# Optimization experiments

Hardware: AMD Instinct MI355X
Metric: run time of the kernel (lower is better)

Reference implementation:

```python
import jax, jax.numpy as jnp
import numpy as np

N = 50000      # nodes
E = 800000     # edges
IN = 128       # in_channels
C = 32         # hidden_channels per head
H = 8          # heads
NC = 2         # num_classes
EPS = 1e-5     # batchnorm eps
SLOPE = 0.2    # leaky relu negative slope


def setup_inputs() -> dict:
    key = jax.random.key(0)
    ks = jax.random.split(key, 16)
    d = {}
    d["x"] = jax.random.normal(ks[0], (N, IN), dtype=jnp.float32)
    d["edge_index"] = jax.random.randint(ks[1], (2, E), 0, N, dtype=jnp.int64)
    # layer 0: IN -> H*C (concat)
    s0 = 1.0 / np.sqrt(IN)
    d["Wl0"] = jax.random.normal(ks[2], (IN, H * C), dtype=jnp.float32) * s0
    d["Wr0"] = jax.random.normal(ks[3], (IN, H * C), dtype=jnp.float32) * s0
    d["att0"] = jax.random.normal(ks[4], (H, C), dtype=jnp.float32) * (1.0 / np.sqrt(C))
    d["b0"] = jnp.zeros((H * C,), dtype=jnp.float32)
    d["g0"] = jnp.ones((H * C,), dtype=jnp.float32)
    d["be0"] = jnp.zeros((H * C,), dtype=jnp.float32)
    d["m0"] = jax.random.normal(ks[5], (H * C,), dtype=jnp.float32) * 0.1
    d["v0"] = jax.random.uniform(ks[6], (H * C,), dtype=jnp.float32, minval=0.5, maxval=1.5)
    # layer 1: H*C -> C (mean over heads, concat=False)
    s1 = 1.0 / np.sqrt(H * C)
    d["Wl1"] = jax.random.normal(ks[7], (H * C, H * C), dtype=jnp.float32) * s1
    d["Wr1"] = jax.random.normal(ks[8], (H * C, H * C), dtype=jnp.float32) * s1
    d["att1"] = jax.random.normal(ks[9], (H, C), dtype=jnp.float32) * (1.0 / np.sqrt(C))
    d["b1"] = jnp.zeros((C,), dtype=jnp.float32)
    d["g1"] = jnp.ones((C,), dtype=jnp.float32)
    d["be1"] = jnp.zeros((C,), dtype=jnp.float32)
    d["m1"] = jax.random.normal(ks[10], (C,), dtype=jnp.float32) * 0.1
    d["v1"] = jax.random.uniform(ks[11], (C,), dtype=jnp.float32, minval=0.5, maxval=1.5)
    # classifier C -> NC
    d["Wc"] = jax.random.normal(ks[12], (C, NC), dtype=jnp.float32) * (1.0 / np.sqrt(C))
    d["bc"] = jnp.zeros((NC,), dtype=jnp.float32)
    return d


def _gatv2_layer(x, src, dst, Wl, Wr, att, b, concat, num_nodes):
    # GATv2Conv (PyG semantics): x_l = source proj, x_r = target proj,
    # e_ij = att . LeakyReLU(x_l[j] + x_r[i]); softmax over incoming edges of i;
    # out_i = sum_j alpha_ij * x_l[j]. Self-loops are added (PyG default).
    nH, nC = att.shape
    xl = (x @ Wl).reshape(num_nodes, nH, nC)
    xr = (x @ Wr).reshape(num_nodes, nH, nC)
    e = xl[src] + xr[dst]                              # [E', H, C]
    e = jnp.where(e > 0, e, SLOPE * e)
    logits = jnp.einsum('ehc,hc->eh', e, att)          # [E', H]
    m = jax.ops.segment_max(logits, dst, num_segments=num_nodes)   # [N, H]
    ex = jnp.exp(logits - m[dst])
    denom = jax.ops.segment_sum(ex, dst, num_segments=num_nodes)   # [N, H]
    alpha = ex / denom[dst]                            # [E', H]
    msg = alpha[:, :, None] * xl[src]                  # [E', H, C]
    out = jax.ops.segment_sum(msg, dst, num_segments=num_nodes)    # [N, H, C]
    if concat:
        return out.reshape(num_nodes, nH * nC) + b
    return out.mean(axis=1) + b


def _bn(x, g, be, m, v):
    return (x - m) * jax.lax.rsqrt(v + EPS) * g + be


def reference(x, edge_index, Wl0, Wr0, att0, b0, g0, be0, m0, v0,
              Wl1, Wr1, att1, b1, g1, be1, m1, v1, Wc, bc):
    num_nodes = x.shape[0]
    loop = jnp.arange(num_nodes, dtype=edge_index.dtype)
    src = jnp.concatenate([edge_index[0], loop])
    dst = jnp.concatenate([edge_index[1], loop])
    h = _gatv2_layer(x, src, dst, Wl0, Wr0, att0, b0, True, num_nodes)
    h = _bn(h, g0, be0, m0, v0)
    h = jax.nn.elu(h)   # eval mode: dropout is identity
    h = _gatv2_layer(h, src, dst, Wl1, Wr1, att1, b1, False, num_nodes)
    h = _bn(h, g1, be1, m1, v1)
    return h @ Wc + bc
```

## Files before the change

kernel.cpp:

```cpp
#include <hip/hip_runtime.h>
#include <math.h>

#define N_NODES 50000
#define M_PAD   50048
#define E_EDGES 800000
#define IN_CH   128
#define C_CH    32
#define H_HEADS 8
#define HC      256
#define BN_EPS  1e-5f
#define SLOPE   0.2f

#define SCAN_CHUNK 512
#define SCAN_B     ((N_NODES + SCAN_CHUNK - 1) / SCAN_CHUNK)

typedef _Float16 f16x8 __attribute__((ext_vector_type(8)));
typedef _Float16 f16x4 __attribute__((ext_vector_type(4)));
typedef _Float16 f16x2 __attribute__((ext_vector_type(2)));
typedef float    f32x4 __attribute__((ext_vector_type(4)));


__global__ void k_init_deg(int* deg, int n) {
    int i = blockIdx.x * blockDim.x + threadIdx.x;
    if (i < n) deg[i] = 1;
}

__global__ void k_hist(const int* __restrict__ dst, int* deg, int e) {
    int i = blockIdx.x * blockDim.x + threadIdx.x;
    if (i < e) atomicAdd(&deg[dst[i]], 1);
}

__global__ __launch_bounds__(256) void k_scan_local(
        const int* __restrict__ deg, int* __restrict__ row_ptr,
        int* __restrict__ partials, int n) {
    __shared__ int sm[256];
    int t = threadIdx.x;
    int base = blockIdx.x * SCAN_CHUNK;
    int i0 = base + 2 * t, i1 = i0 + 1;
    int a = (i0 < n) ? deg[i0] : 0;
    int b = (i1 < n) ? deg[i1] : 0;
    int s = a + b;
    sm[t] = s;
    __syncthreads();
    #pragma unroll
    for (int off = 1; off < 256; off <<= 1) {
        int u = (t >= off) ? sm[t - off] : 0;
        __syncthreads();
        sm[t] += u;
        __syncthreads();
    }
    int excl = sm[t] - s;
    if (i0 < n) row_ptr[i0] = excl;
    if (i1 < n) row_ptr[i1] = excl + a;
    if (t == 255) partials[blockIdx.x] = sm[255];
}

__global__ __launch_bounds__(128) void k_scan_part(
        int* __restrict__ partials, int* __restrict__ row_ptr_n) {
    __shared__ int sm[128];
    int t = threadIdx.x;
    int v = (t < SCAN_B) ? partials[t] : 0;
    sm[t] = v;
    __syncthreads();
    #pragma unroll
    for (int off = 1; off < 128; off <<= 1) {
        int u = (t >= off) ? sm[t - off] : 0;
        __syncthreads();
        sm[t] += u;
        __syncthreads();
    }
    if (t < SCAN_B) partials[t] = sm[t] - v;
    if (t == 127) *row_ptr_n = sm[127];
}

__global__ void k_scan_add(int* __restrict__ row_ptr, int* __restrict__ cursor,
                           const int* __restrict__ partials, int n) {
    int i = blockIdx.x * blockDim.x + threadIdx.x;
    if (i < n) {
        int v = row_ptr[i] + partials[i / SCAN_CHUNK];
        row_ptr[i] = v;
        cursor[i] = v;
    }
}

__global__ void k_fill(const int* __restrict__ src, const int* __restrict__ dst,
                       int* cursor, int* csr_src, int e, int n) {
    int i = blockIdx.x * blockDim.x + threadIdx.x;
    if (i < e) {
        int d = dst[i];
        int p = atomicAdd(&cursor[d], 1);
        csr_src[p] = src[i];
    } else if (i < e + n) {
        int v = i - e;
        int p = atomicAdd(&cursor[v], 1);
        csr_src[p] = v;
    }
}


__global__ void k_split_w4(const float* __restrict__ Wl0, const float* __restrict__ Wr0,
                           const float* __restrict__ Wl1, const float* __restrict__ Wr1,
                           _Float16* __restrict__ W0lt, _Float16* __restrict__ W0rt,
                           _Float16* __restrict__ W1lt, _Float16* __restrict__ W1rt) {
    int t = blockIdx.x * blockDim.x + threadIdx.x;
    const float* W; _Float16* O; int K, rel;
    if (t < 32768)       { W = Wl0; O = W0lt; K = 128; rel = t; }
    else if (t < 65536)  { W = Wr0; O = W0rt; K = 128; rel = t - 32768; }
    else if (t < 131072) { W = Wl1; O = W1lt; K = 256; rel = t - 65536; }
    else if (t < 196608) { W = Wr1; O = W1rt; K = 256; rel = t - 131072; }
    else return;
    int n = rel / K, k = rel - n * K;
    O[rel] = (_Float16)W[(size_t)k * 256 + n];
}


#define BK  32
#define LDA 40

__device__ __forceinline__ f16x8 cvt_h8(float4 a, float4 b) {
    f16x8 v = { (_Float16)a.x, (_Float16)a.y, (_Float16)a.z, (_Float16)a.w,
                (_Float16)b.x, (_Float16)b.y, (_Float16)b.z, (_Float16)b.w };
    return v;
}

__global__ __launch_bounds__(256) void k_gemm_mfma(
        const _Float16* __restrict__ A16, const float* __restrict__ A32,
        const _Float16* __restrict__ W0t, const _Float16* __restrict__ W1t,
        _Float16* __restrict__ C0, _Float16* __restrict__ C1, int K) {
    const _Float16* Wt = blockIdx.z ? W1t : W0t;
    _Float16* C = blockIdx.z ? C1 : C0;
    __shared__ _Float16 As[128 * LDA];
    __shared__ _Float16 Bs[128 * LDA];
    int t = threadIdx.x;
    int lane = t & 63, wv = t >> 6;
    int quad = lane >> 4, r16 = lane & 15;
    size_t mBase = (size_t)blockIdx.x * 128;
    size_t nBase = (size_t)blockIdx.y * 128;
    int sr = t >> 2;
    int sc = (t & 3) * 8;
    f32x4 acc[2][8] = {};
    for (int k0 = 0; k0 < K; k0 += BK) {
        if (A32) {
            size_t r0 = mBase + sr, r1 = r0 + 64;
            float4 a0 = {0.f,0.f,0.f,0.f}, a1 = a0, b0 = a0, b1 = a0;
            if (r0 < N_NODES) {
                const float* g = A32 + r0 * K + k0 + sc;
                a0 = ((const float4*)g)[0];
                a1 = ((const float4*)g)[1];
            }
            if (r1 < N_NODES) {
                const float* g = A32 + r1 * K + k0 + sc;
                b0 = ((const float4*)g)[0];
                b1 = ((const float4*)g)[1];
            }
            *(f16x8*)&As[sr * LDA + sc]        = cvt_h8(a0, a1);
            *(f16x8*)&As[(sr + 64) * LDA + sc] = cvt_h8(b0, b1);
        } else {
            const _Float16* gA = A16 + (mBase + sr) * K + k0 + sc;
            *(f16x8*)&As[sr * LDA + sc]        = *(const f16x8*)gA;
            *(f16x8*)&As[(sr + 64) * LDA + sc] = *(const f16x8*)(gA + (size_t)64 * K);
        }
        const _Float16* gB = Wt + (nBase + sr) * K + k0 + sc;
        *(f16x8*)&Bs[sr * LDA + sc]        = *(const f16x8*)gB;
        *(f16x8*)&Bs[(sr + 64) * LDA + sc] = *(const f16x8*)(gB + (size_t)64 * K);
        __syncthreads();
        f16x8 av[2];
        #pragma unroll
        for (int mi = 0; mi < 2; ++mi) {
            int m = wv * 32 + mi * 16 + r16;
            av[mi] = *(f16x8*)&As[m * LDA + quad * 8];
        }
        #pragma unroll
        for (int ni = 0; ni < 8; ++ni) {
            int n = ni * 16 + r16;
            f16x8 bv = *(f16x8*)&Bs[n * LDA + quad * 8];
            #pragma unroll
            for (int mi = 0; mi < 2; ++mi)
                acc[mi][ni] = __builtin_amdgcn_mfma_f32_16x16x32_f16(av[mi], bv, acc[mi][ni], 0, 0, 0);
        }
        __syncthreads();
    }
    #pragma unroll
    for (int mi = 0; mi < 2; ++mi)
        #pragma unroll
        for (int r = 0; r < 4; ++r) {
            size_t row = mBase + wv * 32 + mi * 16 + quad * 4 + r;
            _Float16* cp = C + row * 256 + nBase + r16;
            #pragma unroll
            for (int ni = 0; ni < 8; ++ni)
                cp[ni * 16] = (_Float16)acc[mi][ni][r];
        }
}


__device__ __forceinline__ float edge_w16(f16x4 h, f16x4 xr, f16x4 att) {
    f16x4 e = h + xr;
    f16x4 es = e * (_Float16)SLOPE;
    f16x4 l = __builtin_elementwise_max(e, es);
#if __has_builtin(__builtin_amdgcn_fdot2)
    f16x2 l01 = __builtin_shufflevector(l, l, 0, 1);
    f16x2 l23 = __builtin_shufflevector(l, l, 2, 3);
    f16x2 a01 = __builtin_shufflevector(att, att, 0, 1);
    f16x2 a23 = __builtin_shufflevector(att, att, 2, 3);
    float p = __builtin_amdgcn_fdot2(l01, a01, 0.f, false);
    p = __builtin_amdgcn_fdot2(l23, a23, p, false);
#else
    float p = (float)l[0] * (float)att[0];
    p = fmaf((float)l[1], (float)att[1], p);
    p = fmaf((float)l[2], (float)att[2], p);
    p = fmaf((float)l[3], (float)att[3], p);
#endif
    p += __shfl_xor(p, 1);
    p += __shfl_xor(p, 2);
    p += __shfl_xor(p, 4);
    return __expf(p);
}

__device__ __forceinline__ float4 edge_accum(
        const f16x4* __restrict__ xl4, f16x4 xr_h, f16x4 att_h,
        const int* __restrict__ csr_src, int beg, int end, int lane) {
    const f16x4* xlp = xl4 + lane;
    float4 acc = {0.f, 0.f, 0.f, 0.f};
    float S = 0.f;
    int j = beg;
    for (; j + 4 <= end; j += 4) {
        int s0 = csr_src[j];
        int s1 = csr_src[j + 1];
        int s2 = csr_src[j + 2];
        int s3 = csr_src[j + 3];
        f16x4 h0 = xlp[(size_t)s0 * 64];
        f16x4 h1 = xlp[(size_t)s1 * 64];
        f16x4 h2 = xlp[(size_t)s2 * 64];
        f16x4 h3 = xlp[(size_t)s3 * 64];
        float w0 = edge_w16(h0, xr_h, att_h);
        float w1 = edge_w16(h1, xr_h, att_h);
        float w2 = edge_w16(h2, xr_h, att_h);
        float w3 = edge_w16(h3, xr_h, att_h);
        S += (w0 + w1) + (w2 + w3);
        acc.x = fmaf((float)h0[0], w0, acc.x); acc.y = fmaf((float)h0[1], w0, acc.y);
        acc.z = fmaf((float)h0[2], w0, acc.z); acc.w = fmaf((float)h0[3], w0, acc.w);
        acc.x = fmaf((float)h1[0], w1, acc.x); acc.y = fmaf((float)h1[1], w1, acc.y);
        acc.z = fmaf((float)h1[2], w1, acc.z); acc.w = fmaf((float)h1[3], w1, acc.w);
        acc.x = fmaf((float)h2[0], w2, acc.x); acc.y = fmaf((float)h2[1], w2, acc.y);
        acc.z = fmaf((float)h2[2], w2, acc.z); acc.w = fmaf((float)h2[3], w2, acc.w);
        acc.x = fmaf((float)h3[0], w3, acc.x); acc.y = fmaf((float)h3[1], w3, acc.y);
        acc.z = fmaf((float)h3[2], w3, acc.z); acc.w = fmaf((float)h3[3], w3, acc.w);
    }
    for (; j < end; ++j) {
        int s = csr_src[j];
        f16x4 hv = xlp[(size_t)s * 64];
        float w = edge_w16(hv, xr_h, att_h);
        S += w;
        acc.x = fmaf((float)hv[0], w, acc.x); acc.y = fmaf((float)hv[1], w, acc.y);
        acc.z = fmaf((float)hv[2], w, acc.z); acc.w = fmaf((float)hv[3], w, acc.w);
    }
    float inv = 1.f / S;
    acc.x *= inv; acc.y *= inv; acc.z *= inv; acc.w *= inv;
    return acc;
}

__device__ __forceinline__ f16x4 cvt_h4(float4 v) {
    f16x4 r = { (_Float16)v.x, (_Float16)v.y, (_Float16)v.z, (_Float16)v.w };
    return r;
}

__global__ __launch_bounds__(256) void k_edge0(
        const _Float16* __restrict__ xl, const _Float16* __restrict__ xr,
        const float* __restrict__ att,
        const int* __restrict__ row_ptr, const int* __restrict__ csr_src,
        const float* __restrict__ b0, const float* __restrict__ g0,
        const float* __restrict__ be0, const float* __restrict__ m0,
        const float* __restrict__ v0,
        _Float16* __restrict__ h0) {
    int lane = threadIdx.x & 63;
    int i = blockIdx.x * 4 + (threadIdx.x >> 6);
    const f16x4* xl4 = (const f16x4*)xl;
    f16x4 xr_h = ((const f16x4*)xr)[(size_t)i * 64 + lane];
    f16x4 att_h = cvt_h4(((const float4*)att)[lane]);
    int beg = row_ptr[i], end = row_ptr[i + 1];
    float4 r = edge_accum(xl4, xr_h, att_h, csr_src, beg, end, lane);
    float4 bb = ((const float4*)b0)[lane];
    float4 gg = ((const float4*)g0)[lane];
    float4 ee = ((const float4*)be0)[lane];
    float4 mm = ((const float4*)m0)[lane];
    float4 vv = ((const float4*)v0)[lane];
    float4 o;
    o.x = (r.x + bb.x - mm.x) * rsqrtf(vv.x + BN_EPS) * gg.x + ee.x;
    o.y = (r.y + bb.y - mm.y) * rsqrtf(vv.y + BN_EPS) * gg.y + ee.y;
    o.z = (r.z + bb.z - mm.z) * rsqrtf(vv.z + BN_EPS) * gg.z + ee.z;
    o.w = (r.w + bb.w - mm.w) * rsqrtf(vv.w + BN_EPS) * gg.w + ee.w;
    o.x = o.x > 0.f ? o.x : expm1f(o.x);
    o.y = o.y > 0.f ? o.y : expm1f(o.y);
    o.z = o.z > 0.f ? o.z : expm1f(o.z);
    o.w = o.w > 0.f ? o.w : expm1f(o.w);
    f16x4 hh = { (_Float16)o.x, (_Float16)o.y, (_Float16)o.z, (_Float16)o.w };
    ((f16x4*)h0)[(size_t)i * 64 + lane] = hh;
}

__global__ __launch_bounds__(256) void k_edge1(
        const _Float16* __restrict__ xl, const _Float16* __restrict__ xr,
        const float* __restrict__ att,
        const int* __restrict__ row_ptr, const int* __restrict__ csr_src,
        const float* __restrict__ b1, const float* __restrict__ g1,
        const float* __restrict__ be1, const float* __restrict__ m1,
        const float* __restrict__ v1,
        const float* __restrict__ Wc, const float* __restrict__ bc,
        float* __restrict__ out) {
    int lane = threadIdx.x & 63;
    int q = lane & 7;
    int i = blockIdx.x * 4 + (threadIdx.x >> 6);
    const f16x4* xl4 = (const f16x4*)xl;
    f16x4 xr_h = ((const f16x4*)xr)[(size_t)i * 64 + lane];
    f16x4 att_h = cvt_h4(((const float4*)att)[lane]);
    int beg = row_ptr[i], end = row_ptr[i + 1];
    float4 r = edge_accum(xl4, xr_h, att_h, csr_src, beg, end, lane);
    #pragma unroll
    for (int mask = 8; mask <= 32; mask <<= 1) {
        r.x += __shfl_xor(r.x, mask);
        r.y += __shfl_xor(r.y, mask);
        r.z += __shfl_xor(r.z, mask);
        r.w += __shfl_xor(r.w, mask);
    }
    float4 bb = ((const float4*)b1)[q];
    float4 gg = ((const float4*)g1)[q];
    float4 ee = ((const float4*)be1)[q];
    float4 mm = ((const float4*)m1)[q];
    float4 vv = ((const float4*)v1)[q];
    r.x = (r.x * 0.125f + bb.x - mm.x) * rsqrtf(vv.x + BN_EPS) * gg.x + ee.x;
    r.y = (r.y * 0.125f + bb.y - mm.y) * rsqrtf(vv.y + BN_EPS) * gg.y + ee.y;
    r.z = (r.z * 0.125f + bb.z - mm.z) * rsqrtf(vv.z + BN_EPS) * gg.z + ee.z;
    r.w = (r.w * 0.125f + bb.w - mm.w) * rsqrtf(vv.w + BN_EPS) * gg.w + ee.w;
    float4 wc0 = ((const float4*)Wc)[q * 2];
    float4 wc1 = ((const float4*)Wc)[q * 2 + 1];
    float o0 = r.x * wc0.x + r.y * wc0.z + r.z * wc1.x + r.w * wc1.z;
    float o1 = r.x * wc0.y + r.y * wc0.w + r.z * wc1.y + r.w * wc1.w;
    #pragma unroll
    for (int mask = 1; mask <= 4; mask <<= 1) {
        o0 += __shfl_xor(o0, mask);
        o1 += __shfl_xor(o1, mask);
    }
    if (lane == 0) {
        float2 ov = {o0 + bc[0], o1 + bc[1]};
        *(float2*)(out + (size_t)i * 2) = ov;
    }
}


extern "C" void kernel_launch(void* const* d_in, const int* in_sizes, int n_in,
                              void* d_out, int out_size, void* d_ws, size_t ws_size,
                              hipStream_t stream) {
    const float* x    = (const float*)d_in[0];
    const int*   ei   = (const int*)d_in[1];
    const float* Wl0  = (const float*)d_in[2];
    const float* Wr0  = (const float*)d_in[3];
    const float* att0 = (const float*)d_in[4];
    const float* b0   = (const float*)d_in[5];
    const float* g0   = (const float*)d_in[6];
    const float* be0  = (const float*)d_in[7];
    const float* m0   = (const float*)d_in[8];
    const float* v0   = (const float*)d_in[9];
    const float* Wl1  = (const float*)d_in[10];
    const float* Wr1  = (const float*)d_in[11];
    const float* att1 = (const float*)d_in[12];
    const float* b1   = (const float*)d_in[13];
    const float* g1   = (const float*)d_in[14];
    const float* be1  = (const float*)d_in[15];
    const float* m1   = (const float*)d_in[16];
    const float* v1   = (const float*)d_in[17];
    const float* Wc   = (const float*)d_in[18];
    const float* bc   = (const float*)d_in[19];
    float* out = (float*)d_out;

    const int N = N_NODES, E = E_EDGES;
    const int* srcp = ei;
    const int* dstp = ei + E;

    char* p = (char*)d_ws;
    _Float16* xlf = (_Float16*)p; p += (size_t)M_PAD * HC * 2;
    _Float16* xrf = (_Float16*)p; p += (size_t)M_PAD * HC * 2;
    _Float16* h0  = (_Float16*)p; p += (size_t)M_PAD * HC * 2;
    _Float16* W0lt = (_Float16*)p; p += (size_t)HC * IN_CH * 2;
    _Float16* W0rt = (_Float16*)p; p += (size_t)HC * IN_CH * 2;
    _Float16* W1lt = (_Float16*)p; p += (size_t)HC * HC * 2;
    _Float16* W1rt = (_Float16*)p; p += (size_t)HC * HC * 2;
    int* deg      = (int*)p;
    int* row_ptr  = deg + N;
    int* cursor   = row_ptr + (N + 1);
    int* partials = cursor + N;
    int* csr_src  = partials + ((SCAN_B + 3) & ~3);

    k_init_deg<<<(N + 255) / 256, 256, 0, stream>>>(deg, N);
    k_hist<<<(E + 255) / 256, 256, 0, stream>>>(dstp, deg, E);
    k_scan_local<<<SCAN_B, 256, 0, stream>>>(deg, row_ptr, partials, N);
    k_scan_part<<<1, 128, 0, stream>>>(partials, row_ptr + N);
    k_scan_add<<<(N + 255) / 256, 256, 0, stream>>>(row_ptr, cursor, partials, N);
    k_fill<<<(E + N + 255) / 256, 256, 0, stream>>>(srcp, dstp, cursor, csr_src, E, N);

    k_split_w4<<<768, 256, 0, stream>>>(Wl0, Wr0, Wl1, Wr1, W0lt, W0rt, W1lt, W1rt);

    dim3 ggrid(M_PAD / 128, 2, 2);
    k_gemm_mfma<<<ggrid, 256, 0, stream>>>(nullptr, x, W0lt, W0rt, xlf, xrf, IN_CH);
    k_edge0<<<N / 4, 256, 0, stream>>>(xlf, xrf, att0, row_ptr, csr_src,
                                       b0, g0, be0, m0, v0, h0);
    k_gemm_mfma<<<ggrid, 256, 0, stream>>>(h0, nullptr, W1lt, W1rt, xlf, xrf, HC);
    k_edge1<<<N / 4, 256, 0, stream>>>(xlf, xrf, att1, row_ptr, csr_src,
                                       b1, g1, be1, m1, v1, Wc, bc, out);
}
```

Baseline: 403.3 us.

## Fuse left/right GEMMs per block, persistent edge kernels, exp2 softmax with folded BN

The GEMM now computes both the left and right projections in one 512-thread block, so each A tile is loaded once and shared by two B tiles. Each wave owns 16 rows instead of 32. The edge kernels become grid-stride persistent loops over a fixed 2048 blocks, with BN scale and shift precomputed once per wave. The exponential switches to a native exp2, with log2e folded into the fp16 attention vector, and per-node index reads go through readfirstlane. Risks are lower per-wave MFMA reuse in the GEMM and small fp16 rounding differences from prescaling the attention vector.

Result: slower. 418.5 us (+3.8%).

```diff
diff --git a/kernel.cpp b/kernel.cpp
--- a/kernel.cpp
+++ b/kernel.cpp
@@ -10,14 +10,24 @@
 #define HC      256
 #define BN_EPS  1e-5f
 #define SLOPE   0.2f
+#define LOG2E   1.44269504f
 
 #define SCAN_CHUNK 512
 #define SCAN_B     ((N_NODES + SCAN_CHUNK - 1) / SCAN_CHUNK)
+
+#define EDGE_BLOCKS 2048
+#define EDGE_WAVES  (EDGE_BLOCKS * 4)
 
 typedef _Float16 f16x8 __attribute__((ext_vector_type(8)));
 typedef _Float16 f16x4 __attribute__((ext_vector_type(4)));
 typedef _Float16 f16x2 __attribute__((ext_vector_type(2)));
 typedef float    f32x4 __attribute__((ext_vector_type(4)));
+
+#if __has_builtin(__builtin_amdgcn_exp2f)
+#define EXP2F(x) __builtin_amdgcn_exp2f(x)
+#else
+#define EXP2F(x) exp2f(x)
+#endif
 
 
 __global__ void k_init_deg(int* deg, int n) {
@@ -123,14 +133,13 @@
     return v;
 }
 
-__global__ __launch_bounds__(256) void k_gemm_mfma(
+__global__ __launch_bounds__(512) void k_gemm_mfma(
         const _Float16* __restrict__ A16, const float* __restrict__ A32,
         const _Float16* __restrict__ W0t, const _Float16* __restrict__ W1t,
         _Float16* __restrict__ C0, _Float16* __restrict__ C1, int K) {
-    const _Float16* Wt = blockIdx.z ? W1t : W0t;
-    _Float16* C = blockIdx.z ? C1 : C0;
-    __shared__ _Float16 As[128 * LDA];
-    __shared__ _Float16 Bs[128 * LDA];
+    __shared__ _Float16 As [128 * LDA];
+    __shared__ _Float16 Bs0[128 * LDA];
+    __shared__ _Float16 Bs1[128 * LDA];
     int t = threadIdx.x;
     int lane = t & 63, wv = t >> 6;
     int quad = lane >> 4, r16 = lane & 15;
@@ -138,58 +147,45 @@
     size_t nBase = (size_t)blockIdx.y * 128;
     int sr = t >> 2;
     int sc = (t & 3) * 8;
-    f32x4 acc[2][8] = {};
+    f32x4 acc0[8] = {}, acc1[8] = {};
     for (int k0 = 0; k0 < K; k0 += BK) {
         if (A32) {
-            size_t r0 = mBase + sr, r1 = r0 + 64;
-            float4 a0 = {0.f,0.f,0.f,0.f}, a1 = a0, b0 = a0, b1 = a0;
+            size_t r0 = mBase + sr;
+            float4 a0 = {0.f, 0.f, 0.f, 0.f}, a1 = a0;
             if (r0 < N_NODES) {
                 const float* g = A32 + r0 * K + k0 + sc;
                 a0 = ((const float4*)g)[0];
                 a1 = ((const float4*)g)[1];
             }
-            if (r1 < N_NODES) {
-                const float* g = A32 + r1 * K + k0 + sc;
-                b0 = ((const float4*)g)[0];
-                b1 = ((const float4*)g)[1];
-            }
-            *(f16x8*)&As[sr * LDA + sc]        = cvt_h8(a0, a1);
-            *(f16x8*)&As[(sr + 64) * LDA + sc] = cvt_h8(b0, b1);
+            *(f16x8*)&As[sr * LDA + sc] = cvt_h8(a0, a1);
         } else {
-            const _Float16* gA = A16 + (mBase + sr) * K + k0 + sc;
-            *(f16x8*)&As[sr * LDA + sc]        = *(const f16x8*)gA;
-            *(f16x8*)&As[(sr + 64) * LDA + sc] = *(const f16x8*)(gA + (size_t)64 * K);
-        }
-        const _Float16* gB = Wt + (nBase + sr) * K + k0 + sc;
-        *(f16x8*)&Bs[sr * LDA + sc]        = *(const f16x8*)gB;
-        *(f16x8*)&Bs[(sr + 64) * LDA + sc] = *(const f16x8*)(gB + (size_t)64 * K);
-        __syncthreads();
-        f16x8 av[2];
-        #pragma unroll
-        for (int mi = 0; mi < 2; ++mi) {
-            int m = wv * 32 + mi * 16 + r16;
-            av[mi] = *(f16x8*)&As[m * LDA + quad * 8];
-        }
+            *(f16x8*)&As[sr * LDA + sc] =
+                *(const f16x8*)(A16 + (size_t)(mBase + sr) * K + k0 + sc);
+        }
+        *(f16x8*)&Bs0[sr * LDA + sc] = *(const f16x8*)(W0t + (size_t)(nBase + sr) * K + k0 + sc);
+        *(f16x8*)&Bs1[sr * LDA + sc] = *(const f16x8*)(W1t + (size_t)(nBase + sr) * K + k0 + sc);
+        __syncthreads();
+        f16x8 av = *(f16x8*)&As[(wv * 16 + r16) * LDA + quad * 8];
         #pragma unroll
         for (int ni = 0; ni < 8; ++ni) {
-            int n = ni * 16 + r16;
-            f16x8 bv = *(f16x8*)&Bs[n * LDA + quad * 8];
-            #pragma unroll
-            for (int mi = 0; mi < 2; ++mi)
-                acc[mi][ni] = __builtin_amdgcn_mfma_f32_16x16x32_f16(av[mi], bv, acc[mi][ni], 0, 0, 0);
+            f16x8 bv0 = *(f16x8*)&Bs0[(ni * 16 + r16) * LDA + quad * 8];
+            f16x8 bv1 = *(f16x8*)&Bs1[(ni * 16 + r16) * LDA + quad * 8];
+            acc0[ni] = __builtin_amdgcn_mfma_f32_16x16x32_f16(av, bv0, acc0[ni], 0, 0, 0);
+            acc1[ni] = __builtin_amdgcn_mfma_f32_16x16x32_f16(av, bv1, acc1[ni], 0, 0, 0);
         }
         __syncthreads();
     }
     #pragma unroll
-    for (int mi = 0; mi < 2; ++mi)
+    for (int r = 0; r < 4; ++r) {
+        size_t row = mBase + wv * 16 + quad * 4 + r;
+        _Float16* cp0 = C0 + row * 256 + nBase + r16;
+        _Float16* cp1 = C1 + row * 256 + nBase + r16;
         #pragma unroll
-        for (int r = 0; r < 4; ++r) {
-            size_t row = mBase + wv * 32 + mi * 16 + quad * 4 + r;
-            _Float16* cp = C + row * 256 + nBase + r16;
-            #pragma unroll
-            for (int ni = 0; ni < 8; ++ni)
-                cp[ni * 16] = (_Float16)acc[mi][ni][r];
-        }
+        for (int ni = 0; ni < 8; ++ni) {
+            cp0[ni * 16] = (_Float16)acc0[ni][r];
+            cp1[ni * 16] = (_Float16)acc1[ni][r];
+        }
+    }
 }
 
 
@@ -213,13 +209,12 @@
     p += __shfl_xor(p, 1);
     p += __shfl_xor(p, 2);
     p += __shfl_xor(p, 4);
-    return __expf(p);
+    return EXP2F(p);
 }
 
 __device__ __forceinline__ float4 edge_accum(
-        const f16x4* __restrict__ xl4, f16x4 xr_h, f16x4 att_h,
-        const int* __restrict__ csr_src, int beg, int end, int lane) {
-    const f16x4* xlp = xl4 + lane;
+        const f16x4* __restrict__ xlp, f16x4 xr_h, f16x4 att_h,
+        const int* __restrict__ csr_src, int beg, int end) {
     float4 acc = {0.f, 0.f, 0.f, 0.f};
     float S = 0.f;
     int j = beg;
@@ -259,11 +254,6 @@
     return acc;
 }
 
-__device__ __forceinline__ f16x4 cvt_h4(float4 v) {
-    f16x4 r = { (_Float16)v.x, (_Float16)v.y, (_Float16)v.z, (_Float16)v.w };
-    return r;
-}
-
 __global__ __launch_bounds__(256) void k_edge0(
         const _Float16* __restrict__ xl, const _Float16* __restrict__ xr,
         const float* __restrict__ att,
@@ -273,28 +263,38 @@
         const float* __restrict__ v0,
         _Float16* __restrict__ h0) {
     int lane = threadIdx.x & 63;
-    int i = blockIdx.x * 4 + (threadIdx.x >> 6);
-    const f16x4* xl4 = (const f16x4*)xl;
-    f16x4 xr_h = ((const f16x4*)xr)[(size_t)i * 64 + lane];
-    f16x4 att_h = cvt_h4(((const float4*)att)[lane]);
-    int beg = row_ptr[i], end = row_ptr[i + 1];
-    float4 r = edge_accum(xl4, xr_h, att_h, csr_src, beg, end, lane);
+    const f16x4* xlp = (const f16x4*)xl + lane;
+    float4 af = ((const float4*)att)[lane];
+    f16x4 att_h = { (_Float16)(af.x * LOG2E), (_Float16)(af.y * LOG2E),
+                    (_Float16)(af.z * LOG2E), (_Float16)(af.w * LOG2E) };
     float4 bb = ((const float4*)b0)[lane];
     float4 gg = ((const float4*)g0)[lane];
     float4 ee = ((const float4*)be0)[lane];
     float4 mm = ((const float4*)m0)[lane];
     float4 vv = ((const float4*)v0)[lane];
-    float4 o;
-    o.x = (r.x + bb.x - mm.x) * rsqrtf(vv.x + BN_EPS) * gg.x + ee.x;
-    o.y = (r.y + bb.y - mm.y) * rsqrtf(vv.y + BN_EPS) * gg.y + ee.y;
-    o.z = (r.z + bb.z - mm.z) * rsqrtf(vv.z + BN_EPS) * gg.z + ee.z;
-    o.w = (r.w + bb.w - mm.w) * rsqrtf(vv.w + BN_EPS) * gg.w + ee.w;
-    o.x = o.x > 0.f ? o.x : expm1f(o.x);
-    o.y = o.y > 0.f ? o.y : expm1f(o.y);
-    o.z = o.z > 0.f ? o.z : expm1f(o.z);
-    o.w = o.w > 0.f ? o.w : expm1f(o.w);
-    f16x4 hh = { (_Float16)o.x, (_Float16)o.y, (_Float16)o.z, (_Float16)o.w };
-    ((f16x4*)h0)[(size_t)i * 64 + lane] = hh;
+    float4 sc, sh;
+    sc.x = rsqrtf(vv.x + BN_EPS) * gg.x;  sh.x = (bb.x - mm.x) * sc.x + ee.x;
+    sc.y = rsqrtf(vv.y + BN_EPS) * gg.y;  sh.y = (bb.y - mm.y) * sc.y + ee.y;
+    sc.z = rsqrtf(vv.z + BN_EPS) * gg.z;  sh.z = (bb.z - mm.z) * sc.z + ee.z;
+    sc.w = rsqrtf(vv.w + BN_EPS) * gg.w;  sh.w = (bb.w - mm.w) * sc.w + ee.w;
+    int w = blockIdx.x * 4 + (threadIdx.x >> 6);
+    for (int i0 = w; i0 < N_NODES; i0 += EDGE_WAVES) {
+        int i = __builtin_amdgcn_readfirstlane(i0);
+        f16x4 xr_h = ((const f16x4*)xr)[(size_t)i * 64 + lane];
+        int beg = row_ptr[i], end = row_ptr[i + 1];
+        float4 r = edge_accum(xlp, xr_h, att_h, csr_src, beg, end);
+        float4 o;
+        o.x = r.x * sc.x + sh.x;
+        o.y = r.y * sc.y + sh.y;
+        o.z = r.z * sc.z + sh.z;
+        o.w = r.w * sc.w + sh.w;
+        o.x = o.x > 0.f ? o.x : expm1f(o.x);
+        o.y = o.y > 0.f ? o.y : expm1f(o.y);
+        o.z = o.z > 0.f ? o.z : expm1f(o.z);
+        o.w = o.w > 0.f ? o.w : expm1f(o.w);
+        f16x4 hh = { (_Float16)o.x, (_Float16)o.y, (_Float16)o.z, (_Float16)o.w };
+        ((f16x4*)h0)[(size_t)i * 64 + lane] = hh;
+    }
 }
 
 __global__ __launch_bounds__(256) void k_edge1(
@@ -308,40 +308,55 @@
         float* __restrict__ out) {
     int lane = threadIdx.x & 63;
     int q = lane & 7;
-    int i = blockIdx.x * 4 + (threadIdx.x >> 6);
-    const f16x4* xl4 = (const f16x4*)xl;
-    f16x4 xr_h = ((const f16x4*)xr)[(size_t)i * 64 + lane];
-    f16x4 att_h = cvt_h4(((const float4*)att)[lane]);
-    int beg = row_ptr[i], end = row_ptr[i + 1];
-    float4 r = edge_accum(xl4, xr_h, att_h, csr_src, beg, end, lane);
-    #pragma unroll
-    for (int mask = 8; mask <= 32; mask <<= 1) {
-        r.x += __shfl_xor(r.x, mask);
-        r.y += __shfl_xor(r.y, mask);
-        r.z += __shfl_xor(r.z, mask);
-        r.w += __shfl_xor(r.w, mask);
-    }
+    const f16x4* xlp = (const f16x4*)xl + lane;
+    float4 af = ((const float4*)att)[lane];
+    f16x4 att_h = { (_Float16)(af.x * LOG2E), (_Float16)(af.y * LOG2E),
+                    (_Float16)(af.z * LOG2E), (_Float16)(af.w * LOG2E) };
     float4 bb = ((const float4*)b1)[q];
     float4 gg = ((const float4*)g1)[q];
     float4 ee = ((const float4*)be1)[q];
     float4 mm = ((const float4*)m1)[q];
     float4 vv = ((const float4*)v1)[q];
-    r.x = (r.x * 0.125f + bb.x - mm.x) * rsqrtf(vv.x + BN_EPS) * gg.x + ee.x;
-    r.y = (r.y * 0.125f + bb.y - mm.y) * rsqrtf(vv.y + BN_EPS) * gg.y + ee.y;
-    r.z = (r.z * 0.125f + bb.z - mm.z) * rsqrtf(vv.z + BN_EPS) * gg.z + ee.z;
-    r.w = (r.w * 0.125f + bb.w - mm.w) * rsqrtf(vv.w + BN_EPS) * gg.w + ee.w;
+    float4 sA, sB;
+    {
+        float s;
+        s = rsqrtf(vv.x + BN_EPS) * gg.x; sA.x = 0.125f * s; sB.x = (bb.x - mm.x) * s + ee.x;
+        s = rsqrtf(vv.y + BN_EPS) * gg.y; sA.y = 0.125f * s; sB.y = (bb.y - mm.y) * s + ee.y;
+        s = rsqrtf(vv.z + BN_EPS) * gg.z; sA.z = 0.125f * s; sB.z = (bb.z - mm.z) * s + ee.z;
+        s = rsqrtf(vv.w + BN_EPS) * gg.w; sA.w = 0.125f * s; sB.w = (bb.w - mm.w) * s + ee.w;
+    }
     float4 wc0 = ((const float4*)Wc)[q * 2];
     float4 wc1 = ((const float4*)Wc)[q * 2 + 1];
-    float o0 = r.x * wc0.x + r.y * wc0.z + r.z * wc1.x + r.w * wc1.z;
-    float o1 = r.x * wc0.y + r.y * wc0.w + r.z * wc1.y + r.w * wc1.w;
-    #pragma unroll
-    for (int mask = 1; mask <= 4; mask <<= 1) {
-        o0 += __shfl_xor(o0, mask);
-        o1 += __shfl_xor(o1, mask);
-    }
-    if (lane == 0) {
-        float2 ov = {o0 + bc[0], o1 + bc[1]};
-        *(float2*)(out + (size_t)i * 2) = ov;
+    float bc0 = bc[0], bc1 = bc[1];
+    int w = blockIdx.x * 4 + (threadIdx.x >> 6);
+    for (int i0 = w; i0 < N_NODES; i0 += EDGE_WAVES) {
+        int i = __builtin_amdgcn_readfirstlane(i0);
+        f16x4 xr_h = ((const f16x4*)xr)[(size_t)i * 64 + lane];
+        int beg = row_ptr[i], end = row_ptr[i + 1];
+        float4 r = edge_accum(xlp, xr_h, att_h, csr_src, beg, end);
+        #pragma unroll
+        for (int mask = 8; mask <= 32; mask <<= 1) {
+            r.x += __shfl_xor(r.x, mask);
+            r.y += __shfl_xor(r.y, mask);
+            r.z += __shfl_xor(r.z, mask);
+            r.w += __shfl_xor(r.w, mask);
+        }
+        float4 o;
+        o.x = r.x * sA.x + sB.x;
+        o.y = r.y * sA.y + sB.y;
+        o.z = r.z * sA.z + sB.z;
+        o.w = r.w * sA.w + sB.w;
+        float o0 = o.x * wc0.x + o.y * wc0.z + o.z * wc1.x + o.w * wc1.z;
+        float o1 = o.x * wc0.y + o.y * wc0.w + o.z * wc1.y + o.w * wc1.w;
+        #pragma unroll
+        for (int mask = 1; mask <= 4; mask <<= 1) {
+            o0 += __shfl_xor(o0, mask);
+            o1 += __shfl_xor(o1, mask);
+        }
+        if (lane == 0) {
+            float2 ov = {o0 + bc0, o1 + bc1};
+            *(float2*)(out + (size_t)i * 2) = ov;
+        }
     }
 }
 
@@ -398,11 +413,11 @@
 
     k_split_w4<<<768, 256, 0, stream>>>(Wl0, Wr0, Wl1, Wr1, W0lt, W0rt, W1lt, W1rt);
 
-    dim3 ggrid(M_PAD / 128, 2, 2);
-    k_gemm_mfma<<<ggrid, 256, 0, stream>>>(nullptr, x, W0lt, W0rt, xlf, xrf, IN_CH);
-    k_edge0<<<N / 4, 256, 0, stream>>>(xlf, xrf, att0, row_ptr, csr_src,
-                                       b0, g0, be0, m0, v0, h0);
-    k_gemm_mfma<<<ggrid, 256, 0, stream>>>(h0, nullptr, W1lt, W1rt, xlf, xrf, HC);
-    k_edge1<<<N / 4, 256, 0, stream>>>(xlf, xrf, att1, row_ptr, csr_src,
-                                       b1, g1, be1, m1, v1, Wc, bc, out);
-}
+    dim3 ggrid(M_PAD / 128, 2);
+    k_gemm_mfma<<<ggrid, 512, 0, stream>>>(nullptr, x, W0lt, W0rt, xlf, xrf, IN_CH);
+    k_edge0<<<EDGE_BLOCKS, 256, 0, stream>>>(xlf, xrf, att0, row_ptr, csr_src,
+                                             b0, g0, be0, m0, v0, h0);
+    k_gemm_mfma<<<ggrid, 512, 0, stream>>>(h0, nullptr, W1lt, W1rt, xlf, xrf, HC);
+    k_edge1<<<EDGE_BLOCKS, 256, 0, stream>>>(xlf, xrf, att1, row_ptr, csr_src,
+                                             b1, g1, be1, m1, v1, Wc, bc, out);
+}
```
